# Optimization experiments

Hardware: AMD Instinct MI355X
Metric: run time of the kernel (lower is better)

Reference implementation:

```python
import jax, jax.numpy as jnp
import numpy as np

NUM_ITER = 3
NUM_SLOTS = 8
SLOT_SIZE = 128
MLP_HIDDEN = 256
EPSILON = 1e-8
INPUT_SIZE = 128
LN_EPS = 1e-5


def layer_norm(x):
    # parameter-free LayerNorm over last dim (LayerNorm() built with no args)
    mu = jnp.mean(x, axis=-1, keepdims=True)
    var = jnp.mean(jnp.square(x - mu), axis=-1, keepdims=True)
    return (x - mu) * jax.lax.rsqrt(var + LN_EPS)


def setup_inputs() -> dict:
    key = jax.random.key(0)
    ks = jax.random.split(key, 16)
    B, N, Din, D, H = 128, 4096, INPUT_SIZE, SLOT_SIZE, MLP_HIDDEN
    s_in = 1.0 / np.sqrt(Din)
    s_d = 1.0 / np.sqrt(D)
    s_h = 1.0 / np.sqrt(H)
    return {
        "inputs": jax.random.normal(ks[0], (B, N, Din), jnp.float32),
        "slots_noise": jax.random.normal(ks[1], (B, NUM_SLOTS, D), jnp.float32),
        "slots_mu": jax.random.normal(ks[2], (1, 1, D), jnp.float32),
        "slots_log_sigma": jax.random.normal(ks[3], (1, 1, D), jnp.float32) * 0.1,
        "Wq": jax.random.normal(ks[4], (D, D), jnp.float32) * s_d,
        "Wk": jax.random.normal(ks[5], (D, Din), jnp.float32) * s_in,
        "Wv": jax.random.normal(ks[6], (D, Din), jnp.float32) * s_in,
        "W_ih": jax.random.normal(ks[7], (3 * D, D), jnp.float32) * s_d,
        "W_hh": jax.random.normal(ks[8], (3 * D, D), jnp.float32) * s_d,
        "b_ih": jax.random.normal(ks[9], (3 * D,), jnp.float32) * s_d,
        "b_hh": jax.random.normal(ks[10], (3 * D,), jnp.float32) * s_d,
        "W1": jax.random.normal(ks[11], (H, D), jnp.float32) * s_d,
        "b1": jnp.zeros((H,), jnp.float32),
        "W2": jax.random.normal(ks[12], (D, H), jnp.float32) * s_h,
        "b2": jnp.zeros((D,), jnp.float32),
    }


def gru_cell(x, h, W_ih, W_hh, b_ih, b_hh):
    # PyTorch GRU, single step. x, h: (..., D)
    gx = x @ W_ih.T + b_ih  # (..., 3D)
    gh = h @ W_hh.T + b_hh
    D = h.shape[-1]
    xr, xz, xn = gx[..., :D], gx[..., D:2 * D], gx[..., 2 * D:]
    hr, hz, hn = gh[..., :D], gh[..., D:2 * D], gh[..., 2 * D:]
    r = jax.nn.sigmoid(xr + hr)
    z = jax.nn.sigmoid(xz + hz)
    n = jnp.tanh(xn + r * hn)
    return (1.0 - z) * n + z * h


def reference(inputs, slots_noise, slots_mu, slots_log_sigma, Wq, Wk, Wv,
              W_ih, W_hh, b_ih, b_hh, W1, b1, W2, b2):
    scale = 1.0 / np.sqrt(SLOT_SIZE)
    x = layer_norm(inputs)                      # (B, N, Din)
    k = x @ Wk.T                                # (B, N, D)
    v = x @ Wv.T                                # (B, N, D)
    slots = slots_mu + jnp.exp(slots_log_sigma) * slots_noise  # (B, S, D)
    for _ in range(NUM_ITER):
        slots_n = layer_norm(slots)             # NOTE: GRU hidden is the NORMED slots (matches source)
        q = slots_n @ Wq.T                      # (B, S, D)
        logits = jnp.einsum("bnd,bsd->bns", k, q) * scale  # (B, N, S)
        attn = jax.nn.softmax(logits, axis=-1) + EPSILON
        attn = attn / jnp.sum(attn, axis=-2, keepdims=True)
        updates = jnp.einsum("bns,bnd->bsd", attn, v)      # (B, S, D)
        slots = gru_cell(updates, slots_n, W_ih, W_hh, b_ih, b_hh)
        slots = slots + (jax.nn.relu(layer_norm(slots) @ W1.T + b1) @ W2.T + b2)
    return slots
```

## Files before the change

### kernel.cpp

```cpp
#include <hip/hip_runtime.h>
#include <math.h>


typedef __attribute__((ext_vector_type(4))) float fx4;
typedef __attribute__((ext_vector_type(8))) short sx8;
typedef __attribute__((ext_vector_type(8))) __bf16 bfx8;

static __device__ __forceinline__ fx4 MFMA(sx8 a, sx8 b, fx4 c) {
  return __builtin_amdgcn_mfma_f32_16x16x32_bf16(
      __builtin_bit_cast(bfx8, a), __builtin_bit_cast(bfx8, b), c, 0, 0, 0);
}

static __device__ __forceinline__ unsigned short f2bf(float f) {
  union { float f; unsigned u; } x; x.f = f;
  unsigned r = x.u + 0x7fffu + ((x.u >> 16) & 1u);
  return (unsigned short)(r >> 16);
}
static __device__ __forceinline__ float bf2f(unsigned short u) {
  union { unsigned u; float f; } x; x.u = ((unsigned)u) << 16; return x.f;
}
static __device__ __forceinline__ fx4 ntload4(const float* p) {
  return __builtin_nontemporal_load((const fx4*)p);
}

#define PST 72

__global__ __launch_bounds__(256) void k_fold(
    const float* __restrict__ Wq, const float* __restrict__ Wk,
    const float* __restrict__ Wih, const float* __restrict__ Wv,
    float* __restrict__ Wqk, float* __restrict__ Wihv) {
  int idx = blockIdx.x * 256 + threadIdx.x;
  if (idx < 16384) {
    int e = idx >> 7, c = idx & 127;
    float s = 0.f;
#pragma unroll 4
    for (int d = 0; d < 128; d++) s += Wq[d * 128 + e] * Wk[d * 128 + c];
    Wqk[idx] = s * 0.08838834764831845f;
    return;
  }
  idx -= 16384;
  if (idx < 49152) {
    int g = idx >> 7, c = idx & 127;
    float s = 0.f;
#pragma unroll 4
    for (int d = 0; d < 128; d++) s += Wih[g * 128 + d] * Wv[d * 128 + c];
    Wihv[idx] = s;
  }
}

__global__ __launch_bounds__(256) void k_pack(
    const float* __restrict__ noise, const float* __restrict__ mu,
    const float* __restrict__ lsig, const float* __restrict__ Wqk,
    const float* __restrict__ Wihv, const float* __restrict__ Whh,
    const float* __restrict__ W1, const float* __restrict__ W2,
    float* __restrict__ slots, unsigned short* __restrict__ wqk_b,
    unsigned short* __restrict__ wihv_b, unsigned short* __restrict__ whh_b,
    unsigned short* __restrict__ w1_b, unsigned short* __restrict__ w2_b) {
  int idx = blockIdx.x * 256 + threadIdx.x;
  if (idx < 131072) {
    int d = idx & 127;
    slots[idx] = mu[d] + expf(lsig[d]) * noise[idx];
    return;
  }
  idx -= 131072;
  if (idx < 16384) {
    wqk_b[idx] = f2bf(Wqk[(idx & 127) * 128 + (idx >> 7)]);
    return;
  }
  idx -= 16384;
  if (idx < 49152) { wihv_b[idx] = f2bf(Wihv[idx]); return; }
  idx -= 49152;
  if (idx < 49152) { whh_b[idx] = f2bf(Whh[idx]); return; }
  idx -= 49152;
  if (idx < 32768) { w1_b[idx] = f2bf(W1[idx]); return; }
  idx -= 32768;
  w2_b[idx] = f2bf(W2[idx]);
}

__global__ __launch_bounds__(64) void k_slot_pre(
    const float* __restrict__ slots, const unsigned short* __restrict__ wqk_b,
    float* __restrict__ slots_n, unsigned short* __restrict__ q2_b) {
  __shared__ __align__(16) short xf[4 * 64 * 8];
  int l = threadIdx.x;
  int r = l & 15, seg = l >> 4;
  long rowbase = (long)blockIdx.x * 16;
  {
    const float* xp = slots + (rowbase + r) * 128 + seg * 32;
    float* snp = slots_n + (rowbase + r) * 128 + seg * 32;
    float v[32];
    float s = 0.f, s2 = 0.f;
#pragma unroll
    for (int i = 0; i < 8; i++) {
      fx4 t = *(const fx4*)(xp + i * 4);
      v[i * 4 + 0] = t.x; v[i * 4 + 1] = t.y; v[i * 4 + 2] = t.z; v[i * 4 + 3] = t.w;
      s += t.x + t.y + t.z + t.w;
      s2 += t.x * t.x + t.y * t.y + t.z * t.z + t.w * t.w;
    }
    s += __shfl_xor(s, 16, 64);  s += __shfl_xor(s, 32, 64);
    s2 += __shfl_xor(s2, 16, 64); s2 += __shfl_xor(s2, 32, 64);
    float mean = s * 0.0078125f;
    float var = s2 * 0.0078125f - mean * mean;
    float rstd = rsqrtf(var + 1e-5f);
#pragma unroll
    for (int i = 0; i < 8; i++) {
      fx4 t = {(v[i * 4 + 0] - mean) * rstd, (v[i * 4 + 1] - mean) * rstd,
               (v[i * 4 + 2] - mean) * rstd, (v[i * 4 + 3] - mean) * rstd};
      *(fx4*)(snp + i * 4) = t;
      v[i * 4 + 0] = t.x; v[i * 4 + 1] = t.y; v[i * 4 + 2] = t.z; v[i * 4 + 3] = t.w;
    }
#pragma unroll
    for (int q = 0; q < 4; q++) {
      sx8 t;
#pragma unroll
      for (int j = 0; j < 8; j++) t[j] = (short)f2bf(v[q * 8 + j]);
      *(sx8*)&xf[(seg * 64 + (r + 16 * q)) * 8] = t;
    }
  }
  __syncthreads();
  const fx4 z4 = {0.f, 0.f, 0.f, 0.f};
  fx4 acc[8];
#pragma unroll
  for (int nt = 0; nt < 8; nt++) acc[nt] = z4;
#pragma unroll
  for (int ks = 0; ks < 4; ks++) {
    sx8 a = *(const sx8*)&xf[(ks * 64 + l) * 8];
#pragma unroll
    for (int nt = 0; nt < 8; nt++) {
      sx8 bfr = *(const sx8*)(wqk_b + (nt * 16 + (l & 15)) * 128 + ks * 32 + (l >> 4) * 8);
      acc[nt] = MFMA(a, bfr, acc[nt]);
    }
  }
  int cl = l & 15, rq = (l >> 4) * 4;
#pragma unroll
  for (int nt = 0; nt < 8; nt++)
#pragma unroll
    for (int rg = 0; rg < 4; rg++)
      q2_b[(rowbase + rq + rg) * 128 + nt * 16 + cl] = f2bf(acc[nt][rg]);
}

__global__ __launch_bounds__(256, 6) void k_attn(
    const unsigned short* __restrict__ ln16, const unsigned short* __restrict__ q2b,
    float* __restrict__ upd_part, float* __restrict__ sattn_part) {
  __shared__ __align__(16) short xlds[64 * 128];
  __shared__ __align__(16) short pplane[2][16 * PST];
  __shared__ float sattnbuf[32];
  int tid = threadIdx.x, w = tid >> 6, l = tid & 63;
  int b = blockIdx.x >> 6, c = blockIdx.x & 63;
  int nr = l & 15, seg = l >> 4, qd = seg * 8;
  int nloc = w * 16 + nr;
  const unsigned short* xt = ln16 + ((long)b * 4096 + c * 64 + nloc) * 128;
  sx8 qf[4];
#pragma unroll
  for (int ks = 0; ks < 4; ks++) {
    if (nr < 8) {
      qf[ks] = *(const sx8*)(q2b + ((long)b * 8 + nr) * 128 + ks * 32 + qd);
    } else {
      sx8 t;
#pragma unroll
      for (int j = 0; j < 8; j++) t[j] = 0;
      qf[ks] = t;
    }
  }
  const fx4 z4 = {0.f, 0.f, 0.f, 0.f};
  fx4 cc = z4;
  int qsw = ((nloc >> 3) & 3) << 5;
#pragma unroll
  for (int ks = 0; ks < 4; ks++) {
    sx8 xr = *(const sx8*)(xt + ks * 32 + qd);
    *(sx8*)&xlds[(nloc * 256 + ((ks * 64 + seg * 16) ^ qsw)) >> 1] = xr;
    cc = MFMA(qf[ks], xr, cc);
  }
  float m01 = fmaxf(fmaxf(cc[0], cc[1]), fmaxf(cc[2], cc[3]));
  m01 = fmaxf(m01, __shfl_xor(m01, 16, 64));
  float p0 = __expf(cc[0] - m01), p1 = __expf(cc[1] - m01),
        p2 = __expf(cc[2] - m01), p3 = __expf(cc[3] - m01);
  float sl = p0 + p1 + p2 + p3;
  sl += __shfl_xor(sl, 16, 64);
  float inv = 1.f / sl;
  float at0 = p0 * inv + 1e-8f, at1 = p1 * inv + 1e-8f;
  float at2 = p2 * inv + 1e-8f, at3 = p3 * inv + 1e-8f;
  {
    unsigned short h0 = f2bf(at0), h1 = f2bf(at1), h2 = f2bf(at2), h3 = f2bf(at3);
    pplane[0][(seg * 4 + 0) * PST + nloc] = (short)h0;
    pplane[0][(seg * 4 + 1) * PST + nloc] = (short)h1;
    pplane[0][(seg * 4 + 2) * PST + nloc] = (short)h2;
    pplane[0][(seg * 4 + 3) * PST + nloc] = (short)h3;
    pplane[1][(seg * 4 + 0) * PST + nloc] = (short)f2bf(at0 - bf2f(h0));
    pplane[1][(seg * 4 + 1) * PST + nloc] = (short)f2bf(at1 - bf2f(h1));
    pplane[1][(seg * 4 + 2) * PST + nloc] = (short)f2bf(at2 - bf2f(h2));
    pplane[1][(seg * 4 + 3) * PST + nloc] = (short)f2bf(at3 - bf2f(h3));
  }
  {
    float v0 = at0, v1 = at1, v2 = at2, v3 = at3;
#pragma unroll
    for (int m = 1; m < 16; m <<= 1) {
      v0 += __shfl_xor(v0, m, 64); v1 += __shfl_xor(v1, m, 64);
      v2 += __shfl_xor(v2, m, 64); v3 += __shfl_xor(v3, m, 64);
    }
    if (nr == 0 && seg < 2) {
      sattnbuf[w * 8 + seg * 4 + 0] = v0;
      sattnbuf[w * 8 + seg * 4 + 1] = v1;
      sattnbuf[w * 8 + seg * 4 + 2] = v2;
      sattnbuf[w * 8 + seg * 4 + 3] = v3;
    }
  }
  __syncthreads();
  fx4 acc[2];
  acc[0] = z4; acc[1] = z4;
#pragma unroll
  for (int nt2 = 0; nt2 < 2; nt2++) {
    int cols = ((((w * 2 + nt2) * 16 + nr) * 2) ^ (seg << 5)) >> 1;
#pragma unroll
    for (int ks2 = 0; ks2 < 2; ks2++) {
      sx8 bfr;
#pragma unroll
      for (int j = 0; j < 8; j++)
        bfr[j] = xlds[(ks2 * 32 + seg * 8 + j) * 128 + cols];
      sx8 pah = *(const sx8*)&pplane[0][nr * PST + ks2 * 32 + seg * 8];
      sx8 pal = *(const sx8*)&pplane[1][nr * PST + ks2 * 32 + seg * 8];
      acc[nt2] = MFMA(pah, bfr, acc[nt2]);
      acc[nt2] = MFMA(pal, bfr, acc[nt2]);
    }
  }
  if (seg < 2) {
    size_t ubase = (size_t)(b * 64 + c) * 1024;
#pragma unroll
    for (int nt2 = 0; nt2 < 2; nt2++)
#pragma unroll
      for (int rg = 0; rg < 4; rg++)
        upd_part[ubase + (seg * 4 + rg) * 128 + (w * 2 + nt2) * 16 + nr] = acc[nt2][rg];
  }
  if (tid < 8)
    sattn_part[(b * 64 + c) * 8 + tid] =
        sattnbuf[tid] + sattnbuf[8 + tid] + sattnbuf[16 + tid] + sattnbuf[24 + tid];
}

__global__ __launch_bounds__(256, 6) void k_attn_first(
    const float* __restrict__ x, unsigned short* __restrict__ ln16,
    const unsigned short* __restrict__ q2b,
    float* __restrict__ upd_part, float* __restrict__ sattn_part) {
  __shared__ __align__(16) short xlds[64 * 128];
  __shared__ __align__(16) short pplane[2][16 * PST];
  __shared__ float sattnbuf[32];
  int tid = threadIdx.x, w = tid >> 6, l = tid & 63;
  int b = blockIdx.x >> 6, c = blockIdx.x & 63;
  int nr = l & 15, seg = l >> 4, qd = seg * 8;
  int nloc = w * 16 + nr;
  long rowg = (long)b * 4096 + c * 64 + nloc;
  const float* xs = x + rowg * 128;
  unsigned short* xo = ln16 + rowg * 128;
  sx8 qf[4];
#pragma unroll
  for (int ks = 0; ks < 4; ks++) {
    if (nr < 8) {
      qf[ks] = *(const sx8*)(q2b + ((long)b * 8 + nr) * 128 + ks * 32 + qd);
    } else {
      sx8 t;
#pragma unroll
      for (int j = 0; j < 8; j++) t[j] = 0;
      qf[ks] = t;
    }
  }
  const fx4 z4 = {0.f, 0.f, 0.f, 0.f};
  float v[32];
  float sm = 0.f, s2 = 0.f;
#pragma unroll
  for (int ks = 0; ks < 4; ks++) {
    fx4 t0 = ntload4(xs + ks * 32 + qd - qd + ks * 0 + ks * 32 + qd * 0 + qd);
    t0 = ntload4(xs + ks * 32 + qd);
    fx4 t1 = ntload4(xs + ks * 32 + qd + 4);
    v[ks * 8 + 0] = t0.x; v[ks * 8 + 1] = t0.y; v[ks * 8 + 2] = t0.z; v[ks * 8 + 3] = t0.w;
    v[ks * 8 + 4] = t1.x; v[ks * 8 + 5] = t1.y; v[ks * 8 + 6] = t1.z; v[ks * 8 + 7] = t1.w;
    sm += t0.x + t0.y + t0.z + t0.w + t1.x + t1.y + t1.z + t1.w;
    s2 += t0.x * t0.x + t0.y * t0.y + t0.z * t0.z + t0.w * t0.w +
          t1.x * t1.x + t1.y * t1.y + t1.z * t1.z + t1.w * t1.w;
  }
  sm += __shfl_xor(sm, 16, 64);  sm += __shfl_xor(sm, 32, 64);
  s2 += __shfl_xor(s2, 16, 64);  s2 += __shfl_xor(s2, 32, 64);
  float mean = sm * 0.0078125f;
  float rstd = rsqrtf(s2 * 0.0078125f - mean * mean + 1e-5f);
  fx4 cc = z4;
  int qsw = ((nloc >> 3) & 3) << 5;
#pragma unroll
  for (int ks = 0; ks < 4; ks++) {
    sx8 t;
#pragma unroll
    for (int j = 0; j < 8; j++) t[j] = (short)f2bf((v[ks * 8 + j] - mean) * rstd);
    *(sx8*)(xo + ks * 32 + qd) = t;
    *(sx8*)&xlds[(nloc * 256 + ((ks * 64 + seg * 16) ^ qsw)) >> 1] = t;
    cc = MFMA(qf[ks], t, cc);
  }
  float m01 = fmaxf(fmaxf(cc[0], cc[1]), fmaxf(cc[2], cc[3]));
  m01 = fmaxf(m01, __shfl_xor(m01, 16, 64));
  float p0 = __expf(cc[0] - m01), p1 = __expf(cc[1] - m01),
        p2 = __expf(cc[2] - m01), p3 = __expf(cc[3] - m01);
  float sl = p0 + p1 + p2 + p3;
  sl += __shfl_xor(sl, 16, 64);
  float inv = 1.f / sl;
  float at0 = p0 * inv + 1e-8f, at1 = p1 * inv + 1e-8f;
  float at2 = p2 * inv + 1e-8f, at3 = p3 * inv + 1e-8f;
  {
    unsigned short h0 = f2bf(at0), h1 = f2bf(at1), h2 = f2bf(at2), h3 = f2bf(at3);
    pplane[0][(seg * 4 + 0) * PST + nloc] = (short)h0;
    pplane[0][(seg * 4 + 1) * PST + nloc] = (short)h1;
    pplane[0][(seg * 4 + 2) * PST + nloc] = (short)h2;
    pplane[0][(seg * 4 + 3) * PST + nloc] = (short)h3;
    pplane[1][(seg * 4 + 0) * PST + nloc] = (short)f2bf(at0 - bf2f(h0));
    pplane[1][(seg * 4 + 1) * PST + nloc] = (short)f2bf(at1 - bf2f(h1));
    pplane[1][(seg * 4 + 2) * PST + nloc] = (short)f2bf(at2 - bf2f(h2));
    pplane[1][(seg * 4 + 3) * PST + nloc] = (short)f2bf(at3 - bf2f(h3));
  }
  {
    float v0 = at0, v1 = at1, v2 = at2, v3 = at3;
#pragma unroll
    for (int m = 1; m < 16; m <<= 1) {
      v0 += __shfl_xor(v0, m, 64); v1 += __shfl_xor(v1, m, 64);
      v2 += __shfl_xor(v2, m, 64); v3 += __shfl_xor(v3, m, 64);
    }
    if (nr == 0 && seg < 2) {
      sattnbuf[w * 8 + seg * 4 + 0] = v0;
      sattnbuf[w * 8 + seg * 4 + 1] = v1;
      sattnbuf[w * 8 + seg * 4 + 2] = v2;
      sattnbuf[w * 8 + seg * 4 + 3] = v3;
    }
  }
  __syncthreads();
  fx4 acc[2];
  acc[0] = z4; acc[1] = z4;
#pragma unroll
  for (int nt2 = 0; nt2 < 2; nt2++) {
    int cols = ((((w * 2 + nt2) * 16 + nr) * 2) ^ (seg << 5)) >> 1;
#pragma unroll
    for (int ks2 = 0; ks2 < 2; ks2++) {
      sx8 bfr;
#pragma unroll
      for (int j = 0; j < 8; j++)
        bfr[j] = xlds[(ks2 * 32 + seg * 8 + j) * 128 + cols];
      sx8 pah = *(const sx8*)&pplane[0][nr * PST + ks2 * 32 + seg * 8];
      sx8 pal = *(const sx8*)&pplane[1][nr * PST + ks2 * 32 + seg * 8];
      acc[nt2] = MFMA(pah, bfr, acc[nt2]);
      acc[nt2] = MFMA(pal, bfr, acc[nt2]);
    }
  }
  if (seg < 2) {
    size_t ubase = (size_t)(b * 64 + c) * 1024;
#pragma unroll
    for (int nt2 = 0; nt2 < 2; nt2++)
#pragma unroll
      for (int rg = 0; rg < 4; rg++)
        upd_part[ubase + (seg * 4 + rg) * 128 + (w * 2 + nt2) * 16 + nr] = acc[nt2][rg];
  }
  if (tid < 8)
    sattn_part[(b * 64 + c) * 8 + tid] =
        sattnbuf[tid] + sattnbuf[8 + tid] + sattnbuf[16 + tid] + sattnbuf[24 + tid];
}

__global__ __launch_bounds__(256) void k_slot_post(
    const float* __restrict__ upd_part, const float* __restrict__ sattn_part,
    float* __restrict__ slots_n,
    const unsigned short* __restrict__ wihv_b, const unsigned short* __restrict__ whh_b,
    const float* __restrict__ b_ih, const float* __restrict__ b_hh,
    const unsigned short* __restrict__ w1_b, const float* __restrict__ b1,
    const unsigned short* __restrict__ w2_b, const float* __restrict__ b2,
    const unsigned short* __restrict__ wqk_b,
    unsigned short* __restrict__ q2_b, float* __restrict__ out_final, int final_flag) {
  __shared__ __align__(16) char smem[78336];
  float* gx = (float*)smem;
  float* gh = (float*)(smem + 24576);
  float* xred = gx;
  short* xfr = (short*)(smem + 49152);
  short* hfr = (short*)(smem + 53248);
  short* ynf = (short*)(smem + 57344);
  short* y1f = (short*)(smem + 61440);
  float* snew = (float*)(smem + 69632);
  float* satred = (float*)(smem + 78080);
  int tid = threadIdx.x, w = tid >> 6, l = tid & 63;
  int rowbase = blockIdx.x * 16;
  int r = l & 15, seg = l >> 4;
  {
    int row = rowbase + r;
    int bb = row >> 3, ss = row & 7;
    float a[32];
#pragma unroll
    for (int i = 0; i < 32; i++) a[i] = 0.f;
    float satsum = 0.f;
#pragma unroll 4
    for (int ci = 0; ci < 16; ci++) {
      int ch = bb * 64 + w * 16 + ci;
      const float* up = upd_part + (size_t)ch * 1024 + ss * 128 + seg * 32;
#pragma unroll
      for (int i = 0; i < 8; i++) {
        fx4 t = *(const fx4*)(up + i * 4);
        a[i * 4 + 0] += t.x; a[i * 4 + 1] += t.y; a[i * 4 + 2] += t.z; a[i * 4 + 3] += t.w;
      }
      satsum += sattn_part[ch * 8 + ss];
    }
#pragma unroll
    for (int i = 0; i < 8; i++) {
      fx4 t = {a[i * 4], a[i * 4 + 1], a[i * 4 + 2], a[i * 4 + 3]};
      *(fx4*)&xred[w * 2048 + r * 128 + seg * 32 + i * 4] = t;
    }
    if (seg == 0) satred[w * 16 + r] = satsum;
  }
  __syncthreads();
  if (w == 0) {
    float inv = 1.f / (satred[r] + satred[16 + r] + satred[32 + r] + satred[48 + r]);
    float a[32];
#pragma unroll
    for (int i = 0; i < 8; i++) {
      fx4 t = *(const fx4*)&xred[r * 128 + seg * 32 + i * 4];
      fx4 t1 = *(const fx4*)&xred[2048 + r * 128 + seg * 32 + i * 4];
      fx4 t2 = *(const fx4*)&xred[4096 + r * 128 + seg * 32 + i * 4];
      fx4 t3 = *(const fx4*)&xred[6144 + r * 128 + seg * 32 + i * 4];
      t = t + t1 + t2 + t3;
      a[i * 4 + 0] = t.x * inv; a[i * 4 + 1] = t.y * inv;
      a[i * 4 + 2] = t.z * inv; a[i * 4 + 3] = t.w * inv;
    }
#pragma unroll
    for (int q = 0; q < 4; q++) {
      sx8 t;
#pragma unroll
      for (int j = 0; j < 8; j++) t[j] = (short)f2bf(a[q * 8 + j]);
      *(sx8*)&xfr[(seg * 64 + (r + 16 * q)) * 8] = t;
    }
  } else if (w == 1) {
    const float* hp = slots_n + (long)(rowbase + r) * 128 + seg * 32;
#pragma unroll
    for (int q = 0; q < 4; q++) {
      fx4 t0 = *(const fx4*)(hp + q * 8);
      fx4 t1 = *(const fx4*)(hp + q * 8 + 4);
      sx8 t;
      t[0] = (short)f2bf(t0.x); t[1] = (short)f2bf(t0.y);
      t[2] = (short)f2bf(t0.z); t[3] = (short)f2bf(t0.w);
      t[4] = (short)f2bf(t1.x); t[5] = (short)f2bf(t1.y);
      t[6] = (short)f2bf(t1.z); t[7] = (short)f2bf(t1.w);
      *(sx8*)&hfr[(seg * 64 + (r + 16 * q)) * 8] = t;
    }
  }
  __syncthreads();
  const fx4 z4 = {0.f, 0.f, 0.f, 0.f};
  {
    fx4 ax[6], ah[6];
#pragma unroll
    for (int j = 0; j < 6; j++) { ax[j] = z4; ah[j] = z4; }
#pragma unroll
    for (int ks = 0; ks < 4; ks++) {
      sx8 a_x = *(const sx8*)&xfr[(ks * 64 + l) * 8];
      sx8 a_h = *(const sx8*)&hfr[(ks * 64 + l) * 8];
#pragma unroll
      for (int j = 0; j < 6; j++) {
        int nt = w * 6 + j;
        sx8 bx = *(const sx8*)(wihv_b + (nt * 16 + (l & 15)) * 128 + ks * 32 + (l >> 4) * 8);
        sx8 bh = *(const sx8*)(whh_b + (nt * 16 + (l & 15)) * 128 + ks * 32 + (l >> 4) * 8);
        ax[j] = MFMA(a_x, bx, ax[j]);
        ah[j] = MFMA(a_h, bh, ah[j]);
      }
    }
#pragma unroll
    for (int j = 0; j < 6; j++) {
      int col = (w * 6 + j) * 16 + (l & 15);
#pragma unroll
      for (int rg = 0; rg < 4; rg++) {
        int row = (l >> 4) * 4 + rg;
        gx[row * 384 + col] = ax[j][rg];
        gh[row * 384 + col] = ah[j][rg];
      }
    }
  }
  __syncthreads();
  {
    int row = tid >> 4, j0 = (tid & 15) * 8;
#pragma unroll
    for (int j = j0; j < j0 + 8; j++) {
      float xr = gx[row * 384 + j] + b_ih[j];
      float xz = gx[row * 384 + 128 + j] + b_ih[128 + j];
      float xn = gx[row * 384 + 256 + j] + b_ih[256 + j];
      float hr = gh[row * 384 + j] + b_hh[j];
      float hz = gh[row * 384 + 128 + j] + b_hh[128 + j];
      float hn = gh[row * 384 + 256 + j] + b_hh[256 + j];
      float rr = 1.f / (1.f + __expf(-(xr + hr)));
      float zz = 1.f / (1.f + __expf(-(xz + hz)));
      float nn = tanhf(xn + rr * hn);
      float h = slots_n[(long)(rowbase + row) * 128 + j];
      snew[row * 132 + j] = (1.f - zz) * nn + zz * h;
    }
  }
  __syncthreads();
  if (w == 0) {
    float v[32];
    float s = 0.f, s2 = 0.f;
#pragma unroll
    for (int i = 0; i < 32; i++) {
      float t = snew[r * 132 + seg * 32 + i];
      v[i] = t; s += t; s2 += t * t;
    }
    s += __shfl_xor(s, 16, 64);  s += __shfl_xor(s, 32, 64);
    s2 += __shfl_xor(s2, 16, 64); s2 += __shfl_xor(s2, 32, 64);
    float mean = s * 0.0078125f;
    float var = s2 * 0.0078125f - mean * mean;
    float rstd = rsqrtf(var + 1e-5f);
#pragma unroll
    for (int q = 0; q < 4; q++) {
      sx8 t;
#pragma unroll
      for (int j = 0; j < 8; j++) t[j] = (short)f2bf((v[q * 8 + j] - mean) * rstd);
      *(sx8*)&ynf[(seg * 64 + (r + 16 * q)) * 8] = t;
    }
  }
  __syncthreads();
  {
    fx4 y[4];
#pragma unroll
    for (int j = 0; j < 4; j++) y[j] = z4;
#pragma unroll
    for (int ks = 0; ks < 4; ks++) {
      sx8 a = *(const sx8*)&ynf[(ks * 64 + l) * 8];
#pragma unroll
      for (int j = 0; j < 4; j++) {
        int nt = w * 4 + j;
        sx8 bf = *(const sx8*)(w1_b + (nt * 16 + (l & 15)) * 128 + ks * 32 + (l >> 4) * 8);
        y[j] = MFMA(a, bf, y[j]);
      }
    }
#pragma unroll
    for (int j = 0; j < 4; j++) {
      int col = (w * 4 + j) * 16 + (l & 15);
      float bias = b1[col];
      int ks3 = col >> 5, qq = (col >> 3) & 3, jj = col & 7;
#pragma unroll
      for (int rg = 0; rg < 4; rg++) {
        float val = fmaxf(y[j][rg] + bias, 0.f);
        int m = (l >> 4) * 4 + rg;
        y1f[(ks3 * 64 + m + 16 * qq) * 8 + jj] = (short)f2bf(val);
      }
    }
  }
  __syncthreads();
  {
    fx4 zz2[2];
    zz2[0] = z4; zz2[1] = z4;
#pragma unroll
    for (int ks = 0; ks < 8; ks++) {
      sx8 a = *(const sx8*)&y1f[(ks * 64 + l) * 8];
#pragma unroll
      for (int j = 0; j < 2; j++) {
        sx8 bf = *(const sx8*)(w2_b + ((w * 2 + j) * 16 + (l & 15)) * 256 + ks * 32 + (l >> 4) * 8);
        zz2[j] = MFMA(a, bf, zz2[j]);
      }
    }
#pragma unroll
    for (int j = 0; j < 2; j++) {
      int col = (w * 2 + j) * 16 + (l & 15);
      float bias = b2[col];
#pragma unroll
      for (int rg = 0; rg < 4; rg++) {
        int row = (l >> 4) * 4 + rg;
        snew[row * 132 + col] += zz2[j][rg] + bias;
      }
    }
  }
  __syncthreads();
  if (final_flag) {
    int row = tid >> 4, c8 = (tid & 15) * 8;
    fx4 t0 = *(const fx4*)&snew[row * 132 + c8];
    fx4 t1 = *(const fx4*)&snew[row * 132 + c8 + 4];
    *(fx4*)(out_final + (long)(rowbase + row) * 128 + c8) = t0;
    *(fx4*)(out_final + (long)(rowbase + row) * 128 + c8 + 4) = t1;
    return;
  }
  if (w == 0) {
    float v[32];
    float s = 0.f, s2 = 0.f;
#pragma unroll
    for (int i = 0; i < 32; i++) {
      float t = snew[r * 132 + seg * 32 + i];
      v[i] = t; s += t; s2 += t * t;
    }
    s += __shfl_xor(s, 16, 64);  s += __shfl_xor(s, 32, 64);
    s2 += __shfl_xor(s2, 16, 64); s2 += __shfl_xor(s2, 32, 64);
    float mean = s * 0.0078125f;
    float var = s2 * 0.0078125f - mean * mean;
    float rstd = rsqrtf(var + 1e-5f);
    float* snp = slots_n + (long)(rowbase + r) * 128 + seg * 32;
#pragma unroll
    for (int i = 0; i < 8; i++) {
      fx4 t = {(v[i * 4 + 0] - mean) * rstd, (v[i * 4 + 1] - mean) * rstd,
               (v[i * 4 + 2] - mean) * rstd, (v[i * 4 + 3] - mean) * rstd};
      *(fx4*)(snp + i * 4) = t;
      v[i * 4 + 0] = t.x; v[i * 4 + 1] = t.y; v[i * 4 + 2] = t.z; v[i * 4 + 3] = t.w;
    }
#pragma unroll
    for (int q = 0; q < 4; q++) {
      sx8 t;
#pragma unroll
      for (int j = 0; j < 8; j++) t[j] = (short)f2bf(v[q * 8 + j]);
      *(sx8*)&ynf[(seg * 64 + (r + 16 * q)) * 8] = t;
    }
  }
  __syncthreads();
  {
    fx4 acc2[2];
    acc2[0] = z4; acc2[1] = z4;
#pragma unroll
    for (int ks = 0; ks < 4; ks++) {
      sx8 a = *(const sx8*)&ynf[(ks * 64 + l) * 8];
#pragma unroll
      for (int j = 0; j < 2; j++) {
        int nt = w * 2 + j;
        sx8 bf = *(const sx8*)(wqk_b + (nt * 16 + (l & 15)) * 128 + ks * 32 + (l >> 4) * 8);
        acc2[j] = MFMA(a, bf, acc2[j]);
      }
    }
    int cl = l & 15, rq = (l >> 4) * 4;
#pragma unroll
    for (int j = 0; j < 2; j++) {
      int nt = w * 2 + j;
#pragma unroll
      for (int rg = 0; rg < 4; rg++)
        q2_b[(long)(rowbase + rq + rg) * 128 + nt * 16 + cl] = f2bf(acc2[j][rg]);
    }
  }
}

extern "C" void kernel_launch(void* const* d_in, const int* in_sizes, int n_in,
                              void* d_out, int out_size, void* d_ws, size_t ws_size,
                              hipStream_t stream) {
  (void)in_sizes; (void)n_in; (void)out_size; (void)ws_size;
  const float* x = (const float*)d_in[0];
  const float* noise = (const float*)d_in[1];
  const float* mu = (const float*)d_in[2];
  const float* lsig = (const float*)d_in[3];
  const float* Wq = (const float*)d_in[4];
  const float* Wk = (const float*)d_in[5];
  const float* Wv = (const float*)d_in[6];
  const float* Wih = (const float*)d_in[7];
  const float* Whh = (const float*)d_in[8];
  const float* b_ih = (const float*)d_in[9];
  const float* b_hh = (const float*)d_in[10];
  const float* W1 = (const float*)d_in[11];
  const float* b1 = (const float*)d_in[12];
  const float* W2 = (const float*)d_in[13];
  const float* b2 = (const float*)d_in[14];

  char* ws = (char*)d_ws;
  size_t off = 0;
  auto take = [&](size_t bytes) {
    char* p = ws + off;
    off += (bytes + 255) & ~(size_t)255;
    return p;
  };
  unsigned short* ln16 = (unsigned short*)take(134217728);
  float* Wqk = (float*)take(65536);
  float* Wihv = (float*)take(196608);
  unsigned short* wqk_b = (unsigned short*)take(32768);
  unsigned short* wihv_b = (unsigned short*)take(98304);
  unsigned short* whh_b = (unsigned short*)take(98304);
  unsigned short* w1_b = (unsigned short*)take(65536);
  unsigned short* w2_b = (unsigned short*)take(65536);
  float* slots = (float*)take(524288);
  float* slots_n = (float*)take(524288);
  unsigned short* q2_b = (unsigned short*)take(262144);
  float* upd_part = (float*)take(33554432);
  float* sattn_part = (float*)take(262144);

  k_fold<<<256, 256, 0, stream>>>(Wq, Wk, Wih, Wv, Wqk, Wihv);
  k_pack<<<1216, 256, 0, stream>>>(noise, mu, lsig, Wqk, Wihv, Whh, W1, W2,
                                   slots, wqk_b, wihv_b, whh_b, w1_b, w2_b);
  k_slot_pre<<<64, 64, 0, stream>>>(slots, wqk_b, slots_n, q2_b);
  k_attn_first<<<8192, 256, 0, stream>>>(x, ln16, q2_b, upd_part, sattn_part);
  k_slot_post<<<64, 256, 0, stream>>>(upd_part, sattn_part, slots_n, wihv_b, whh_b,
                                      b_ih, b_hh, w1_b, b1, w2_b, b2, wqk_b,
                                      q2_b, (float*)d_out, 0);
  for (int it = 1; it < 3; it++) {
    k_attn<<<8192, 256, 0, stream>>>(ln16, q2_b, upd_part, sattn_part);
    k_slot_post<<<64, 256, 0, stream>>>(upd_part, sattn_part, slots_n, wihv_b, whh_b,
                                        b_ih, b_hh, w1_b, b1, w2_b, b2, wqk_b,
                                        q2_b, (float*)d_out, (it == 2) ? 1 : 0);
  }
}
```

Before: 593.5 us.

## Process four token chunks per attention block with double-buffered LDS pipeline

```diff
diff --git a/kernel.cpp b/kernel.cpp
--- a/kernel.cpp
+++ b/kernel.cpp
@@ -24,6 +24,29 @@
 }
 
 #define PST 72
+
+static __device__ __forceinline__ void softmax_store(
+    fx4 cc, float* satacc, short* ph, short* pl, int nloc, int seg) {
+  float m01 = fmaxf(fmaxf(cc[0], cc[1]), fmaxf(cc[2], cc[3]));
+  m01 = fmaxf(m01, __shfl_xor(m01, 16, 64));
+  float p0 = __expf(cc[0] - m01), p1 = __expf(cc[1] - m01),
+        p2 = __expf(cc[2] - m01), p3 = __expf(cc[3] - m01);
+  float sl = p0 + p1 + p2 + p3;
+  sl += __shfl_xor(sl, 16, 64);
+  float inv = 1.f / sl;
+  float at0 = p0 * inv + 1e-8f, at1 = p1 * inv + 1e-8f;
+  float at2 = p2 * inv + 1e-8f, at3 = p3 * inv + 1e-8f;
+  satacc[0] += at0; satacc[1] += at1; satacc[2] += at2; satacc[3] += at3;
+  unsigned short h0 = f2bf(at0), h1 = f2bf(at1), h2 = f2bf(at2), h3 = f2bf(at3);
+  ph[(seg * 4 + 0) * PST + nloc] = (short)h0;
+  ph[(seg * 4 + 1) * PST + nloc] = (short)h1;
+  ph[(seg * 4 + 2) * PST + nloc] = (short)h2;
+  ph[(seg * 4 + 3) * PST + nloc] = (short)h3;
+  pl[(seg * 4 + 0) * PST + nloc] = (short)f2bf(at0 - bf2f(h0));
+  pl[(seg * 4 + 1) * PST + nloc] = (short)f2bf(at1 - bf2f(h1));
+  pl[(seg * 4 + 2) * PST + nloc] = (short)f2bf(at2 - bf2f(h2));
+  pl[(seg * 4 + 3) * PST + nloc] = (short)f2bf(at3 - bf2f(h3));
+}
 
 __global__ __launch_bounds__(256) void k_fold(
     const float* __restrict__ Wq, const float* __restrict__ Wk,
@@ -138,17 +161,17 @@
       q2_b[(rowbase + rq + rg) * 128 + nt * 16 + cl] = f2bf(acc[nt][rg]);
 }
 
-__global__ __launch_bounds__(256, 6) void k_attn(
+__global__ __launch_bounds__(256, 3) void k_attn(
     const unsigned short* __restrict__ ln16, const unsigned short* __restrict__ q2b,
     float* __restrict__ upd_part, float* __restrict__ sattn_part) {
-  __shared__ __align__(16) short xlds[64 * 128];
-  __shared__ __align__(16) short pplane[2][16 * PST];
+  __shared__ __align__(16) short xlds[2][64 * 128];
+  __shared__ __align__(16) short pplane[2][2][16 * PST];
   __shared__ float sattnbuf[32];
   int tid = threadIdx.x, w = tid >> 6, l = tid & 63;
-  int b = blockIdx.x >> 6, c = blockIdx.x & 63;
+  int b = blockIdx.x >> 4, c = blockIdx.x & 15;
   int nr = l & 15, seg = l >> 4, qd = seg * 8;
   int nloc = w * 16 + nr;
-  const unsigned short* xt = ln16 + ((long)b * 4096 + c * 64 + nloc) * 128;
+  const unsigned short* xt = ln16 + ((long)b * 4096 + c * 256 + nloc) * 128;
   sx8 qf[4];
 #pragma unroll
   for (int ks = 0; ks < 4; ks++) {
@@ -162,36 +185,67 @@
     }
   }
   const fx4 z4 = {0.f, 0.f, 0.f, 0.f};
-  fx4 cc = z4;
+  float satacc[4] = {0.f, 0.f, 0.f, 0.f};
+  fx4 acc[2];
+  acc[0] = z4; acc[1] = z4;
   int qsw = ((nloc >> 3) & 3) << 5;
-#pragma unroll
-  for (int ks = 0; ks < 4; ks++) {
-    sx8 xr = *(const sx8*)(xt + ks * 32 + qd);
-    *(sx8*)&xlds[(nloc * 256 + ((ks * 64 + seg * 16) ^ qsw)) >> 1] = xr;
-    cc = MFMA(qf[ks], xr, cc);
-  }
-  float m01 = fmaxf(fmaxf(cc[0], cc[1]), fmaxf(cc[2], cc[3]));
-  m01 = fmaxf(m01, __shfl_xor(m01, 16, 64));
-  float p0 = __expf(cc[0] - m01), p1 = __expf(cc[1] - m01),
-        p2 = __expf(cc[2] - m01), p3 = __expf(cc[3] - m01);
-  float sl = p0 + p1 + p2 + p3;
-  sl += __shfl_xor(sl, 16, 64);
-  float inv = 1.f / sl;
-  float at0 = p0 * inv + 1e-8f, at1 = p1 * inv + 1e-8f;
-  float at2 = p2 * inv + 1e-8f, at3 = p3 * inv + 1e-8f;
-  {
-    unsigned short h0 = f2bf(at0), h1 = f2bf(at1), h2 = f2bf(at2), h3 = f2bf(at3);
-    pplane[0][(seg * 4 + 0) * PST + nloc] = (short)h0;
-    pplane[0][(seg * 4 + 1) * PST + nloc] = (short)h1;
-    pplane[0][(seg * 4 + 2) * PST + nloc] = (short)h2;
-    pplane[0][(seg * 4 + 3) * PST + nloc] = (short)h3;
-    pplane[1][(seg * 4 + 0) * PST + nloc] = (short)f2bf(at0 - bf2f(h0));
-    pplane[1][(seg * 4 + 1) * PST + nloc] = (short)f2bf(at1 - bf2f(h1));
-    pplane[1][(seg * 4 + 2) * PST + nloc] = (short)f2bf(at2 - bf2f(h2));
-    pplane[1][(seg * 4 + 3) * PST + nloc] = (short)f2bf(at3 - bf2f(h3));
-  }
-  {
-    float v0 = at0, v1 = at1, v2 = at2, v3 = at3;
+  sx8 xr[4];
+#pragma unroll
+  for (int ks = 0; ks < 4; ks++) xr[ks] = *(const sx8*)(xt + ks * 32 + qd);
+  {
+    fx4 cc = z4;
+#pragma unroll
+    for (int ks = 0; ks < 4; ks++) {
+      *(sx8*)&xlds[0][(nloc * 256 + ((ks * 64 + seg * 16) ^ qsw)) >> 1] = xr[ks];
+      cc = MFMA(qf[ks], xr[ks], cc);
+    }
+    softmax_store(cc, satacc, &pplane[0][0][0], &pplane[0][1][0], nloc, seg);
+  }
+  __syncthreads();
+#pragma unroll
+  for (int t = 0; t < 4; t++) {
+    if (t < 3) {
+#pragma unroll
+      for (int ks = 0; ks < 4; ks++)
+        xr[ks] = *(const sx8*)(xt + (t + 1) * 8192 + ks * 32 + qd);
+    }
+#pragma unroll
+    for (int nt2 = 0; nt2 < 2; nt2++) {
+      int cols = ((((w * 2 + nt2) * 16 + nr) * 2) ^ (seg << 5)) >> 1;
+#pragma unroll
+      for (int ks2 = 0; ks2 < 2; ks2++) {
+        sx8 bfr;
+#pragma unroll
+        for (int j = 0; j < 8; j++)
+          bfr[j] = xlds[t & 1][(ks2 * 32 + seg * 8 + j) * 128 + cols];
+        sx8 pah = *(const sx8*)&pplane[t & 1][0][nr * PST + ks2 * 32 + seg * 8];
+        sx8 pal = *(const sx8*)&pplane[t & 1][1][nr * PST + ks2 * 32 + seg * 8];
+        acc[nt2] = MFMA(pah, bfr, acc[nt2]);
+        acc[nt2] = MFMA(pal, bfr, acc[nt2]);
+      }
+    }
+    if (t < 3) {
+      fx4 cc = z4;
+#pragma unroll
+      for (int ks = 0; ks < 4; ks++) {
+        *(sx8*)&xlds[(t + 1) & 1][(nloc * 256 + ((ks * 64 + seg * 16) ^ qsw)) >> 1] = xr[ks];
+        cc = MFMA(qf[ks], xr[ks], cc);
+      }
+      softmax_store(cc, satacc, &pplane[(t + 1) & 1][0][0], &pplane[(t + 1) & 1][1][0],
+                    nloc, seg);
+      __syncthreads();
+    }
+  }
+  if (seg < 2) {
+    size_t ubase = (size_t)(b * 16 + c) * 1024;
+#pragma unroll
+    for (int nt2 = 0; nt2 < 2; nt2++)
+#pragma unroll
+      for (int rg = 0; rg < 4; rg++)
+        upd_part[ubase + (seg * 4 + rg) * 128 + (w * 2 + nt2) * 16 + nr] = acc[nt2][rg];
+  }
+  {
+    float v0 = satacc[0], v1 = satacc[1], v2 = satacc[2], v3 = satacc[3];
 #pragma unroll
     for (int m = 1; m < 16; m <<= 1) {
       v0 += __shfl_xor(v0, m, 64); v1 += __shfl_xor(v1, m, 64);
@@ -205,48 +259,23 @@
     }
   }
   __syncthreads();
-  fx4 acc[2];
-  acc[0] = z4; acc[1] = z4;
-#pragma unroll
-  for (int nt2 = 0; nt2 < 2; nt2++) {
-    int cols = ((((w * 2 + nt2) * 16 + nr) * 2) ^ (seg << 5)) >> 1;
-#pragma unroll
-    for (int ks2 = 0; ks2 < 2; ks2++) {
-      sx8 bfr;
-#pragma unroll
-      for (int j = 0; j < 8; j++)
-        bfr[j] = xlds[(ks2 * 32 + seg * 8 + j) * 128 + cols];
-      sx8 pah = *(const sx8*)&pplane[0][nr * PST + ks2 * 32 + seg * 8];
-      sx8 pal = *(const sx8*)&pplane[1][nr * PST + ks2 * 32 + seg * 8];
-      acc[nt2] = MFMA(pah, bfr, acc[nt2]);
-      acc[nt2] = MFMA(pal, bfr, acc[nt2]);
-    }
-  }
-  if (seg < 2) {
-    size_t ubase = (size_t)(b * 64 + c) * 1024;
-#pragma unroll
-    for (int nt2 = 0; nt2 < 2; nt2++)
-#pragma unroll
-      for (int rg = 0; rg < 4; rg++)
-        upd_part[ubase + (seg * 4 + rg) * 128 + (w * 2 + nt2) * 16 + nr] = acc[nt2][rg];
-  }
   if (tid < 8)
-    sattn_part[(b * 64 + c) * 8 + tid] =
+    sattn_part[(b * 16 + c) * 8 + tid] =
         sattnbuf[tid] + sattnbuf[8 + tid] + sattnbuf[16 + tid] + sattnbuf[24 + tid];
 }
 
-__global__ __launch_bounds__(256, 6) void k_attn_first(
+__global__ __launch_bounds__(256, 3) void k_attn_first(
     const float* __restrict__ x, unsigned short* __restrict__ ln16,
     const unsigned short* __restrict__ q2b,
     float* __restrict__ upd_part, float* __restrict__ sattn_part) {
-  __shared__ __align__(16) short xlds[64 * 128];
-  __shared__ __align__(16) short pplane[2][16 * PST];
+  __shared__ __align__(16) short xlds[2][64 * 128];
+  __shared__ __align__(16) short pplane[2][2][16 * PST];
   __shared__ float sattnbuf[32];
   int tid = threadIdx.x, w = tid >> 6, l = tid & 63;
-  int b = blockIdx.x >> 6, c = blockIdx.x & 63;
+  int b = blockIdx.x >> 4, c = blockIdx.x & 15;
   int nr = l & 15, seg = l >> 4, qd = seg * 8;
   int nloc = w * 16 + nr;
-  long rowg = (long)b * 4096 + c * 64 + nloc;
+  long rowg = (long)b * 4096 + c * 256 + nloc;
   const float* xs = x + rowg * 128;
   unsigned short* xo = ln16 + rowg * 128;
   sx8 qf[4];
@@ -262,56 +291,99 @@
     }
   }
   const fx4 z4 = {0.f, 0.f, 0.f, 0.f};
-  float v[32];
-  float sm = 0.f, s2 = 0.f;
-#pragma unroll
-  for (int ks = 0; ks < 4; ks++) {
-    fx4 t0 = ntload4(xs + ks * 32 + qd - qd + ks * 0 + ks * 32 + qd * 0 + qd);
-    t0 = ntload4(xs + ks * 32 + qd);
-    fx4 t1 = ntload4(xs + ks * 32 + qd + 4);
-    v[ks * 8 + 0] = t0.x; v[ks * 8 + 1] = t0.y; v[ks * 8 + 2] = t0.z; v[ks * 8 + 3] = t0.w;
-    v[ks * 8 + 4] = t1.x; v[ks * 8 + 5] = t1.y; v[ks * 8 + 6] = t1.z; v[ks * 8 + 7] = t1.w;
-    sm += t0.x + t0.y + t0.z + t0.w + t1.x + t1.y + t1.z + t1.w;
-    s2 += t0.x * t0.x + t0.y * t0.y + t0.z * t0.z + t0.w * t0.w +
-          t1.x * t1.x + t1.y * t1.y + t1.z * t1.z + t1.w * t1.w;
-  }
-  sm += __shfl_xor(sm, 16, 64);  sm += __shfl_xor(sm, 32, 64);
-  s2 += __shfl_xor(s2, 16, 64);  s2 += __shfl_xor(s2, 32, 64);
-  float mean = sm * 0.0078125f;
-  float rstd = rsqrtf(s2 * 0.0078125f - mean * mean + 1e-5f);
-  fx4 cc = z4;
+  float satacc[4] = {0.f, 0.f, 0.f, 0.f};
+  fx4 acc[2];
+  acc[0] = z4; acc[1] = z4;
   int qsw = ((nloc >> 3) & 3) << 5;
-#pragma unroll
-  for (int ks = 0; ks < 4; ks++) {
-    sx8 t;
-#pragma unroll
-    for (int j = 0; j < 8; j++) t[j] = (short)f2bf((v[ks * 8 + j] - mean) * rstd);
-    *(sx8*)(xo + ks * 32 + qd) = t;
-    *(sx8*)&xlds[(nloc * 256 + ((ks * 64 + seg * 16) ^ qsw)) >> 1] = t;
-    cc = MFMA(qf[ks], t, cc);
-  }
-  float m01 = fmaxf(fmaxf(cc[0], cc[1]), fmaxf(cc[2], cc[3]));
-  m01 = fmaxf(m01, __shfl_xor(m01, 16, 64));
-  float p0 = __expf(cc[0] - m01), p1 = __expf(cc[1] - m01),
-        p2 = __expf(cc[2] - m01), p3 = __expf(cc[3] - m01);
-  float sl = p0 + p1 + p2 + p3;
-  sl += __shfl_xor(sl, 16, 64);
-  float inv = 1.f / sl;
-  float at0 = p0 * inv + 1e-8f, at1 = p1 * inv + 1e-8f;
-  float at2 = p2 * inv + 1e-8f, at3 = p3 * inv + 1e-8f;
-  {
-    unsigned short h0 = f2bf(at0), h1 = f2bf(at1), h2 = f2bf(at2), h3 = f2bf(at3);
-    pplane[0][(seg * 4 + 0) * PST + nloc] = (short)h0;
-    pplane[0][(seg * 4 + 1) * PST + nloc] = (short)h1;
-    pplane[0][(seg * 4 + 2) * PST + nloc] = (short)h2;
-    pplane[0][(seg * 4 + 3) * PST + nloc] = (short)h3;
-    pplane[1][(seg * 4 + 0) * PST + nloc] = (short)f2bf(at0 - bf2f(h0));
-    pplane[1][(seg * 4 + 1) * PST + nloc] = (short)f2bf(at1 - bf2f(h1));
-    pplane[1][(seg * 4 + 2) * PST + nloc] = (short)f2bf(at2 - bf2f(h2));
-    pplane[1][(seg * 4 + 3) * PST + nloc] = (short)f2bf(at3 - bf2f(h3));
-  }
-  {
-    float v0 = at0, v1 = at1, v2 = at2, v3 = at3;
+  fx4 vn[8];
+#pragma unroll
+  for (int i = 0; i < 8; i++) vn[i] = ntload4(xs + (i >> 1) * 32 + qd + (i & 1) * 4);
+  {
+    float sm = 0.f, s2 = 0.f;
+#pragma unroll
+    for (int i = 0; i < 8; i++) {
+      fx4 t = vn[i];
+      sm += t.x + t.y + t.z + t.w;
+      s2 += t.x * t.x + t.y * t.y + t.z * t.z + t.w * t.w;
+    }
+    sm += __shfl_xor(sm, 16, 64);  sm += __shfl_xor(sm, 32, 64);
+    s2 += __shfl_xor(s2, 16, 64);  s2 += __shfl_xor(s2, 32, 64);
+    float mean = sm * 0.0078125f;
+    float rstd = rsqrtf(s2 * 0.0078125f - mean * mean + 1e-5f);
+    fx4 cc = z4;
+#pragma unroll
+    for (int ks = 0; ks < 4; ks++) {
+      sx8 t;
+#pragma unroll
+      for (int j = 0; j < 8; j++)
+        t[j] = (short)f2bf((vn[ks * 2 + (j >> 2)][j & 3] - mean) * rstd);
+      *(sx8*)(xo + ks * 32 + qd) = t;
+      *(sx8*)&xlds[0][(nloc * 256 + ((ks * 64 + seg * 16) ^ qsw)) >> 1] = t;
+      cc = MFMA(qf[ks], t, cc);
+    }
+    softmax_store(cc, satacc, &pplane[0][0][0], &pplane[0][1][0], nloc, seg);
+  }
+  __syncthreads();
+#pragma unroll
+  for (int t = 0; t < 4; t++) {
+    if (t < 3) {
+#pragma unroll
+      for (int i = 0; i < 8; i++)
+        vn[i] = ntload4(xs + (t + 1) * 8192 + (i >> 1) * 32 + qd + (i & 1) * 4);
+    }
+#pragma unroll
+    for (int nt2 = 0; nt2 < 2; nt2++) {
+      int cols = ((((w * 2 + nt2) * 16 + nr) * 2) ^ (seg << 5)) >> 1;
+#pragma unroll
+      for (int ks2 = 0; ks2 < 2; ks2++) {
+        sx8 bfr;
+#pragma unroll
+        for (int j = 0; j < 8; j++)
+          bfr[j] = xlds[t & 1][(ks2 * 32 + seg * 8 + j) * 128 + cols];
+        sx8 pah = *(const sx8*)&pplane[t & 1][0][nr * PST + ks2 * 32 + seg * 8];
+        sx8 pal = *(const sx8*)&pplane[t & 1][1][nr * PST + ks2 * 32 + seg * 8];
+        acc[nt2] = MFMA(pah, bfr, acc[nt2]);
+        acc[nt2] = MFMA(pal, bfr, acc[nt2]);
+      }
+    }
+    if (t < 3) {
+      float sm = 0.f, s2 = 0.f;
+#pragma unroll
+      for (int i = 0; i < 8; i++) {
+        fx4 tt = vn[i];
+        sm += tt.x + tt.y + tt.z + tt.w;
+        s2 += tt.x * tt.x + tt.y * tt.y + tt.z * tt.z + tt.w * tt.w;
+      }
+      sm += __shfl_xor(sm, 16, 64);  sm += __shfl_xor(sm, 32, 64);
+      s2 += __shfl_xor(s2, 16, 64);  s2 += __shfl_xor(s2, 32, 64);
+      float mean = sm * 0.0078125f;
+      float rstd = rsqrtf(s2 * 0.0078125f - mean * mean + 1e-5f);
+      fx4 cc = z4;
+#pragma unroll
+      for (int ks = 0; ks < 4; ks++) {
+        sx8 tt;
+#pragma unroll
+        for (int j = 0; j < 8; j++)
+          tt[j] = (short)f2bf((vn[ks * 2 + (j >> 2)][j & 3] - mean) * rstd);
+        *(sx8*)(xo + (t + 1) * 8192 + ks * 32 + qd) = tt;
+        *(sx8*)&xlds[(t + 1) & 1][(nloc * 256 + ((ks * 64 + seg * 16) ^ qsw)) >> 1] = tt;
+        cc = MFMA(qf[ks], tt, cc);
+      }
+      softmax_store(cc, satacc, &pplane[(t + 1) & 1][0][0], &pplane[(t + 1) & 1][1][0],
+                    nloc, seg);
+      __syncthreads();
+    }
+  }
+  if (seg < 2) {
+    size_t ubase = (size_t)(b * 16 + c) * 1024;
+#pragma unroll
+    for (int nt2 = 0; nt2 < 2; nt2++)
+#pragma unroll
+      for (int rg = 0; rg < 4; rg++)
+        upd_part[ubase + (seg * 4 + rg) * 128 + (w * 2 + nt2) * 16 + nr] = acc[nt2][rg];
+  }
+  {
+    float v0 = satacc[0], v1 = satacc[1], v2 = satacc[2], v3 = satacc[3];
 #pragma unroll
     for (int m = 1; m < 16; m <<= 1) {
       v0 += __shfl_xor(v0, m, 64); v1 += __shfl_xor(v1, m, 64);
@@ -325,33 +397,8 @@
     }
   }
   __syncthreads();
-  fx4 acc[2];
-  acc[0] = z4; acc[1] = z4;
-#pragma unroll
-  for (int nt2 = 0; nt2 < 2; nt2++) {
-    int cols = ((((w * 2 + nt2) * 16 + nr) * 2) ^ (seg << 5)) >> 1;
-#pragma unroll
-    for (int ks2 = 0; ks2 < 2; ks2++) {
-      sx8 bfr;
-#pragma unroll
-      for (int j = 0; j < 8; j++)
-        bfr[j] = xlds[(ks2 * 32 + seg * 8 + j) * 128 + cols];
-      sx8 pah = *(const sx8*)&pplane[0][nr * PST + ks2 * 32 + seg * 8];
-      sx8 pal = *(const sx8*)&pplane[1][nr * PST + ks2 * 32 + seg * 8];
-      acc[nt2] = MFMA(pah, bfr, acc[nt2]);
-      acc[nt2] = MFMA(pal, bfr, acc[nt2]);
-    }
-  }
-  if (seg < 2) {
-    size_t ubase = (size_t)(b * 64 + c) * 1024;
-#pragma unroll
-    for (int nt2 = 0; nt2 < 2; nt2++)
-#pragma unroll
-      for (int rg = 0; rg < 4; rg++)
-        upd_part[ubase + (seg * 4 + rg) * 128 + (w * 2 + nt2) * 16 + nr] = acc[nt2][rg];
-  }
   if (tid < 8)
-    sattn_part[(b * 64 + c) * 8 + tid] =
+    sattn_part[(b * 16 + c) * 8 + tid] =
         sattnbuf[tid] + sattnbuf[8 + tid] + sattnbuf[16 + tid] + sattnbuf[24 + tid];
 }
 
@@ -384,9 +431,9 @@
 #pragma unroll
     for (int i = 0; i < 32; i++) a[i] = 0.f;
     float satsum = 0.f;
-#pragma unroll 4
-    for (int ci = 0; ci < 16; ci++) {
-      int ch = bb * 64 + w * 16 + ci;
+#pragma unroll
+    for (int ci = 0; ci < 4; ci++) {
+      int ch = bb * 16 + w * 4 + ci;
       const float* up = upd_part + (size_t)ch * 1024 + ss * 128 + seg * 32;
 #pragma unroll
       for (int i = 0; i < 8; i++) {
@@ -660,19 +707,19 @@
   float* slots = (float*)take(524288);
   float* slots_n = (float*)take(524288);
   unsigned short* q2_b = (unsigned short*)take(262144);
-  float* upd_part = (float*)take(33554432);
-  float* sattn_part = (float*)take(262144);
+  float* upd_part = (float*)take(8388608);
+  float* sattn_part = (float*)take(65536);
 
   k_fold<<<256, 256, 0, stream>>>(Wq, Wk, Wih, Wv, Wqk, Wihv);
   k_pack<<<1216, 256, 0, stream>>>(noise, mu, lsig, Wqk, Wihv, Whh, W1, W2,
                                    slots, wqk_b, wihv_b, whh_b, w1_b, w2_b);
   k_slot_pre<<<64, 64, 0, stream>>>(slots, wqk_b, slots_n, q2_b);
-  k_attn_first<<<8192, 256, 0, stream>>>(x, ln16, q2_b, upd_part, sattn_part);
+  k_attn_first<<<2048, 256, 0, stream>>>(x, ln16, q2_b, upd_part, sattn_part);
   k_slot_post<<<64, 256, 0, stream>>>(upd_part, sattn_part, slots_n, wihv_b, whh_b,
                                       b_ih, b_hh, w1_b, b1, w2_b, b2, wqk_b,
                                       q2_b, (float*)d_out, 0);
   for (int it = 1; it < 3; it++) {
-    k_attn<<<8192, 256, 0, stream>>>(ln16, q2_b, upd_part, sattn_part);
+    k_attn<<<2048, 256, 0, stream>>>(ln16, q2_b, upd_part, sattn_part);
     k_slot_post<<<64, 256, 0, stream>>>(upd_part, sattn_part, slots_n, wihv_b, whh_b,
                                         b_ih, b_hh, w1_b, b1, w2_b, b2, wqk_b,
                                         q2_b, (float*)d_out, (it == 2) ? 1 : 0);
```

Result: faster. 549.3 us (-7.4%).
